# Kernel tuning notes

Hardware: AMD Instinct MI355X
Metric: run time of the kernel (lower is better)

Reference implementation:

```python
import jax, jax.numpy as jnp
import numpy as np

N = 50000
E = 800000
D = 128
H = 8
DH = D // H


def setup_inputs() -> dict:
    key = jax.random.key(0)
    ks = jax.random.split(key, 8)
    x = jax.random.normal(ks[0], (N, D), dtype=jnp.float32)
    src = jax.random.randint(ks[1], (E,), 0, N, dtype=jnp.int32)
    dst = jax.random.randint(ks[2], (E,), 0, N, dtype=jnp.int32)
    s = 1.0 / np.sqrt(D)
    w_qkv = jax.random.uniform(ks[3], (3 * D, D), jnp.float32, -s, s)
    b_qkv = jax.random.uniform(ks[4], (3 * D,), jnp.float32, -s, s)
    w_out = jax.random.uniform(ks[5], (D, D), jnp.float32, -s, s)
    b_out = jax.random.uniform(ks[6], (D,), jnp.float32, -s, s)
    return {"x": x, "src": src, "dst": dst, "w_qkv": w_qkv, "b_qkv": b_qkv,
            "w_out": w_out, "b_out": b_out}


def reference(x, src, dst, w_qkv, b_qkv, w_out, b_out):
    n = x.shape[0]
    coef = 1.0 / np.sqrt(DH)
    qkv = (x @ w_qkv.T + b_qkv).reshape(n, H, 3 * DH)
    q, k, v = qkv[..., :DH], qkv[..., DH:2 * DH], qkv[..., 2 * DH:]
    # per-edge scores: dot(k[src], q[dst]) per head -> [E, H]
    scores = jnp.einsum('ehd,ehd->eh', k[src], q[dst]) * coef
    # edge softmax over edges sharing the same destination node
    smax = jax.ops.segment_max(scores, dst, num_segments=n)  # [N, H]
    smax = jnp.where(jnp.isfinite(smax), smax, 0.0)
    ex = jnp.exp(scores - smax[dst])                          # [E, H]
    denom = jax.ops.segment_sum(ex, dst, num_segments=n)      # [N, H]
    probs = ex / jnp.maximum(denom[dst], 1e-30)
    # weighted aggregation of source values -> [N, H, DH]
    agg = jax.ops.segment_sum(probs[:, :, None] * v[src], dst, num_segments=n)
    out = agg.reshape(n, D) @ w_out.T + b_out
    return out
```

## Files before the change

kernel.cpp:

```cpp
#include <hip/hip_runtime.h>
#include <math.h>

#define DD   128
#define NQKV 384
#define CAP  128

typedef __attribute__((ext_vector_type(8))) short          bf16x8;
typedef __attribute__((ext_vector_type(8))) unsigned short ushort8;
typedef __attribute__((ext_vector_type(4))) float          f32x4;

__device__ __forceinline__ unsigned short f2bf(float f) {
    unsigned u = __float_as_uint(f);
    u += 0x7fffu + ((u >> 16) & 1u);
    return (unsigned short)(u >> 16);
}
__device__ __forceinline__ float bflo(unsigned u) { return __uint_as_float(u << 16); }
__device__ __forceinline__ float bfhi(unsigned u) { return __uint_as_float(u & 0xffff0000u); }

__device__ __forceinline__ unsigned char f2e4m3(float f) {
    float a = f * 0x1p-120f;
    unsigned u = __float_as_uint(a);
    unsigned s = (u >> 24) & 0x80u;
    u &= 0x7fffffffu;
    u += 0x7ffffu + ((u >> 20) & 1u);
    unsigned mag = u >> 20;
    if (mag > 0x7eu) mag = 0x7eu;
    return (unsigned char)(s | mag);
}
__device__ __forceinline__ float e4m3f(unsigned w, int k) {
    unsigned t = w << (24 - 8 * k);
    return __uint_as_float((t & 0x80000000u) | ((t & 0x7f000000u) >> 4));
}

#define NWQ8 (NQKV * DD / 8)
#define NWO8 (DD * DD / 8)

__global__ void prep_kernel(const float* __restrict__ x,
                            const float* __restrict__ w_qkv, const float* __restrict__ w_out,
                            unsigned short* __restrict__ xbf,
                            unsigned short* __restrict__ wqb, unsigned short* __restrict__ wob,
                            int* __restrict__ counts, int nzc4, int nx8) {
    int i = blockIdx.x * blockDim.x + threadIdx.x;
    if (i < nzc4) {
        ((int4*)counts)[i] = make_int4(0, 0, 0, 0);
        return;
    }
    int j = i - nzc4;
    const float* s;
    unsigned short* d;
    if (j < NWQ8)              { s = w_qkv + (size_t)j * 8; d = wqb + (size_t)j * 8; }
    else if (j < NWQ8 + NWO8)  { int k = j - NWQ8; s = w_out + (size_t)k * 8; d = wob + (size_t)k * 8; }
    else {
        int k = j - NWQ8 - NWO8;
        if (k >= nx8) return;
        s = x + (size_t)k * 8; d = xbf + (size_t)k * 8;
    }
    const float4* p = (const float4*)s;
    float4 a = p[0], b = p[1];
    float v[8] = {a.x, a.y, a.z, a.w, b.x, b.y, b.z, b.w};
    ushort8 vh;
    #pragma unroll
    for (int t = 0; t < 8; ++t) vh[t] = f2bf(v[t]);
    *(ushort8*)d = vh;
}

#define TM 128
#define TN 128
#define GY_QKV 170
#define GX_OUT 196

__global__ __launch_bounds__(256, 2) void scatter_qkv_kernel(
    const int* __restrict__ src, const int* __restrict__ dst,
    int* __restrict__ counts, int* __restrict__ lists, int E, int nsb,
    const unsigned short* __restrict__ Xb,
    const unsigned short* __restrict__ B,
    const float* __restrict__ bias, unsigned short* __restrict__ Cq,
    unsigned char* __restrict__ Ck8, unsigned short* __restrict__ Cv,
    int M, int mtiles)
{
    __shared__ unsigned short Bs[TN * DD];

    if ((int)blockIdx.x < nsb) {
        int t = blockIdx.x * blockDim.x + threadIdx.x;
        int base = t * 8;
        if (base >= E) return;
        if (base + 8 <= E) {
            int4 d0 = *(const int4*)(dst + base);
            int4 d1 = *(const int4*)(dst + base + 4);
            int4 s0 = *(const int4*)(src + base);
            int4 s1 = *(const int4*)(src + base + 4);
            int dd[8] = {d0.x, d0.y, d0.z, d0.w, d1.x, d1.y, d1.z, d1.w};
            int ss[8] = {s0.x, s0.y, s0.z, s0.w, s1.x, s1.y, s1.z, s1.w};
            int pos[8];
            #pragma unroll
            for (int i = 0; i < 8; ++i) pos[i] = atomicAdd(&counts[dd[i]], 1);
            #pragma unroll
            for (int i = 0; i < 8; ++i)
                if (pos[i] < CAP) lists[(size_t)dd[i] * CAP + pos[i]] = ss[i];
        } else {
            for (int e = base; e < E; ++e) {
                int d = dst[e];
                int pos = atomicAdd(&counts[d], 1);
                if (pos < CAP) lists[(size_t)d * CAP + pos] = src[e];
            }
        }
        return;
    }

    const int qb   = (int)blockIdx.x - nsb;
    const int tid  = threadIdx.x;
    const int l    = tid & 63;
    const int wv   = tid >> 6;
    const int quad = l >> 4;
    const int l15  = l & 15;
    const int wm   = (wv & 1) * 64;
    const int wn   = (wv >> 1) * 64;
    const int n0   = (qb % 3) * TN;
    const int mt_start = qb / 3;

    const size_t gbase = (size_t)n0 * DD;
    for (int i = tid; i < TN * 16; i += 256) {
        int col = i >> 4, g = i & 15;
        int gs  = g ^ (col & 15);
        *(ushort8*)&Bs[col * DD + gs * 8] = *(const ushort8*)(B + gbase + (size_t)col * DD + g * 8);
    }
    __syncthreads();

    for (int mt0 = mt_start; mt0 < mtiles; mt0 += GY_QKV) {
        const int m0 = mt0 * TM;

        f32x4 acc[4][4];
        #pragma unroll
        for (int i = 0; i < 4; ++i)
            #pragma unroll
            for (int j = 0; j < 4; ++j) acc[i][j] = (f32x4)0.f;

        bf16x8 af[4][4];
        #pragma unroll
        for (int mt = 0; mt < 4; ++mt) {
            const unsigned short* ar = Xb + (size_t)(m0 + wm + mt * 16 + l15) * DD + quad * 8;
            #pragma unroll
            for (int kq = 0; kq < 4; ++kq) af[mt][kq] = *(const bf16x8*)(ar + kq * 32);
        }

        #pragma unroll
        for (int kq = 0; kq < 4; ++kq) {
            bf16x8 bh[4];
            #pragma unroll
            for (int nt = 0; nt < 4; ++nt) {
                int colL = wn + nt * 16 + l15;
                int gs   = (kq * 4 + quad) ^ (colL & 15);
                bh[nt] = *(const bf16x8*)&Bs[colL * DD + gs * 8];
            }
            #pragma unroll
            for (int mt = 0; mt < 4; ++mt)
                #pragma unroll
                for (int nt = 0; nt < 4; ++nt)
                    acc[mt][nt] = __builtin_amdgcn_mfma_f32_16x16x32_bf16(af[mt][kq], bh[nt], acc[mt][nt], 0, 0, 0);
        }

        #pragma unroll
        for (int nt = 0; nt < 4; ++nt) {
            int j = n0 + wn + nt * 16 + l15;
            float bj = bias[j];
            int h = j / 48;
            int r = j - h * 48;
            int seg = (r >= 32) ? 2 : ((r >= 16) ? 1 : 0);
            int bc  = h * 16 + r - seg * 16;
            if (seg == 1) {
                #pragma unroll
                for (int mt = 0; mt < 4; ++mt)
                    #pragma unroll
                    for (int rr = 0; rr < 4; ++rr) {
                        int m = m0 + wm + mt * 16 + quad * 4 + rr;
                        if (m < M) Ck8[(size_t)m * DD + bc] = f2e4m3(acc[mt][nt][rr] + bj);
                    }
            } else {
                unsigned short* dstp = (seg == 0 ? Cq : Cv);
                #pragma unroll
                for (int mt = 0; mt < 4; ++mt)
                    #pragma unroll
                    for (int rr = 0; rr < 4; ++rr) {
                        int m = m0 + wm + mt * 16 + quad * 4 + rr;
                        if (m < M) dstp[(size_t)m * DD + bc] = f2bf(acc[mt][nt][rr] + bj);
                    }
            }
        }
    }
}

__global__ __launch_bounds__(256, 2) void out_gemm_kernel(
    const unsigned short* __restrict__ A,
    const unsigned short* __restrict__ B,
    const float* __restrict__ bias, float* __restrict__ C, int M, int mtiles)
{
    __shared__ unsigned short Bs[TN * DD];

    const int tid  = threadIdx.x;
    const int l    = tid & 63;
    const int wv   = tid >> 6;
    const int quad = l >> 4;
    const int l15  = l & 15;
    const int wm   = (wv & 1) * 64;
    const int wn   = (wv >> 1) * 64;

    for (int i = tid; i < TN * 16; i += 256) {
        int col = i >> 4, g = i & 15;
        int gs  = g ^ (col & 15);
        *(ushort8*)&Bs[col * DD + gs * 8] = *(const ushort8*)(B + (size_t)col * DD + g * 8);
    }
    __syncthreads();

    for (int mt0 = blockIdx.x; mt0 < mtiles; mt0 += gridDim.x) {
        const int m0 = mt0 * TM;

        f32x4 acc[4][4];
        #pragma unroll
        for (int i = 0; i < 4; ++i)
            #pragma unroll
            for (int j = 0; j < 4; ++j) acc[i][j] = (f32x4)0.f;

        bf16x8 af[4][4];
        #pragma unroll
        for (int mt = 0; mt < 4; ++mt) {
            const int mrow = m0 + wm + mt * 16 + l15;
            const int mclamp = (mrow < M) ? mrow : (M - 1);
            #pragma unroll
            for (int kq = 0; kq < 4; ++kq)
                af[mt][kq] = *(const bf16x8*)(A + (size_t)mclamp * DD + kq * 32 + quad * 8);
        }

        #pragma unroll
        for (int kq = 0; kq < 4; ++kq) {
            bf16x8 bh[4];
            #pragma unroll
            for (int nt = 0; nt < 4; ++nt) {
                int colL = wn + nt * 16 + l15;
                int gs   = (kq * 4 + quad) ^ (colL & 15);
                bh[nt] = *(const bf16x8*)&Bs[colL * DD + gs * 8];
            }
            #pragma unroll
            for (int mt = 0; mt < 4; ++mt)
                #pragma unroll
                for (int nt = 0; nt < 4; ++nt)
                    acc[mt][nt] = __builtin_amdgcn_mfma_f32_16x16x32_bf16(af[mt][kq], bh[nt], acc[mt][nt], 0, 0, 0);
        }

        #pragma unroll
        for (int nt = 0; nt < 4; ++nt) {
            int j = wn + nt * 16 + l15;
            float bj = bias[j];
            #pragma unroll
            for (int mt = 0; mt < 4; ++mt)
                #pragma unroll
                for (int rr = 0; rr < 4; ++rr) {
                    int m = m0 + wm + mt * 16 + quad * 4 + rr;
                    if (m < M) C[(size_t)m * DD + j] = acc[mt][nt][rr] + bj;
                }
        }
    }
}

#define ATTN_BLOCKS 2048

#define ATTN_STEP(cka, cvv, nka, nvv)                                             \
  {                                                                                \
    const int cnt  = min(8, deg - c);                                              \
    const bool more = (c + 8 < deg);                                               \
    const int nn = lists[row0 + min(c + 16 + e, deg - 1)];                         \
    if (more) {                                                                    \
      nka = *(const uint4*)(kb8 + ((((unsigned)nxt) << 7) + hoff));                \
      _Pragma("unroll")                                                            \
      for (int ee = 0; ee < 8; ++ee)                                               \
        nvv[ee] = *(const unsigned*)(vb8 + ((((unsigned)__shfl(nxt, ee)) << 8) + loff4)); \
    }                                                                              \
         \
    float sA = e4m3f(cka.x, 0) * q0.x;                                             \
    sA = fmaf(e4m3f(cka.x, 1), q0.y, sA);                                          \
    sA = fmaf(e4m3f(cka.x, 2), q0.z, sA);                                          \
    sA = fmaf(e4m3f(cka.x, 3), q0.w, sA);                                          \
    float sB = e4m3f(cka.y, 0) * q1.x;                                             \
    sB = fmaf(e4m3f(cka.y, 1), q1.y, sB);                                          \
    sB = fmaf(e4m3f(cka.y, 2), q1.z, sB);                                          \
    sB = fmaf(e4m3f(cka.y, 3), q1.w, sB);                                          \
    float sC = e4m3f(cka.z, 0) * q2.x;                                             \
    sC = fmaf(e4m3f(cka.z, 1), q2.y, sC);                                          \
    sC = fmaf(e4m3f(cka.z, 2), q2.z, sC);                                          \
    sC = fmaf(e4m3f(cka.z, 3), q2.w, sC);                                          \
    float sD = e4m3f(cka.w, 0) * q3.x;                                             \
    sD = fmaf(e4m3f(cka.w, 1), q3.y, sD);                                          \
    sD = fmaf(e4m3f(cka.w, 2), q3.z, sD);                                          \
    sD = fmaf(e4m3f(cka.w, 3), q3.w, sD);                                          \
    const float s_ = (sA + sB) + (sC + sD);                                        \
    const float pp = __expf(s_ * 0.25f);                           \
    const float p_ = (e < cnt) ? pp : 0.f;                                         \
    l_run += p_;                                                                   \
    _Pragma("unroll")                                                              \
    for (int ee = 0; ee < 8; ++ee) {                                               \
      const float pe = __shfl(p_, lbase | ee);          \
      if ((ee & 1) == 0) {                                                         \
        acc0a = fmaf(pe, bflo(cvv[ee]), acc0a);                                    \
        acc1a = fmaf(pe, bfhi(cvv[ee]), acc1a);                                    \
      } else {                                                                     \
        acc0b = fmaf(pe, bflo(cvv[ee]), acc0b);                                    \
        acc1b = fmaf(pe, bfhi(cvv[ee]), acc1b);                                    \
      }                                                                            \
    }                                                                              \
    nxt = nn;                                                                      \
    c += 8;                                                                        \
  }

__global__ __launch_bounds__(256) void wave_attn_kernel(
    const unsigned short* __restrict__ qbf, const unsigned char* __restrict__ k8,
    const unsigned short* __restrict__ vbf, const int* __restrict__ lists,
    const int* __restrict__ counts,
    unsigned short* __restrict__ agg, int N)
{
    const int lane   = threadIdx.x & 63;
    const int wid    = blockIdx.x * 4 + (threadIdx.x >> 6);
    const int nwaves = gridDim.x * 4;

    const int h = lane >> 3;
    const int e = lane & 7;
    const unsigned hoff  = (unsigned)h << 4;
    const unsigned loff4 = (unsigned)lane << 2;
    const int lbase = lane & 0x38;

    const char* kb8 = (const char*)k8;
    const char* vb8 = (const char*)vbf;
    const char* qb8 = (const char*)qbf;
    char*       ab8 = (char*)agg;

    for (int n = wid; n < N; n += nwaves) {
        const int deg = min(counts[n], CAP);
        const unsigned ooff = (((unsigned)n) << 8) + loff4;
        if (deg == 0) {
            *(unsigned*)(ab8 + ooff) = 0u;
            continue;
        }

        const int row0 = n * CAP;

        const unsigned qoff = (((unsigned)n) << 8) + ((unsigned)h << 5);
        const uint4 qa = *(const uint4*)(qb8 + qoff);
        const uint4 qb = *(const uint4*)(qb8 + qoff + 16);
        const float S = 0x1p120f;
        const float4 q0 = make_float4(bflo(qa.x)*S, bfhi(qa.x)*S, bflo(qa.y)*S, bfhi(qa.y)*S);
        const float4 q1 = make_float4(bflo(qa.z)*S, bfhi(qa.z)*S, bflo(qa.w)*S, bfhi(qa.w)*S);
        const float4 q2 = make_float4(bflo(qb.x)*S, bfhi(qb.x)*S, bflo(qb.y)*S, bfhi(qb.y)*S);
        const float4 q3 = make_float4(bflo(qb.z)*S, bfhi(qb.z)*S, bflo(qb.w)*S, bfhi(qb.w)*S);

        const int c0s = lists[row0 + min(e, deg - 1)];
        int nxt = lists[row0 + min(8 + e, deg - 1)];

        uint4 ka0, ka1;
        unsigned vv0[8], vv1[8];
        {
            ka0 = *(const uint4*)(kb8 + ((((unsigned)c0s) << 7) + hoff));
            #pragma unroll
            for (int ee = 0; ee < 8; ++ee)
                vv0[ee] = *(const unsigned*)(vb8 + ((((unsigned)__shfl(c0s, ee)) << 8) + loff4));
        }
        ka1 = ka0;
        #pragma unroll
        for (int ee = 0; ee < 8; ++ee) vv1[ee] = 0u;

        float l_run = 0.f;
        float acc0a = 0.f, acc0b = 0.f, acc1a = 0.f, acc1b = 0.f;

        int c = 0;
        for (;;) {
            ATTN_STEP(ka0, vv0, ka1, vv1);
            if (c >= deg) break;
            ATTN_STEP(ka1, vv1, ka0, vv0);
            if (c >= deg) break;
        }

        l_run += __shfl_xor(l_run, 1);
        l_run += __shfl_xor(l_run, 2);
        l_run += __shfl_xor(l_run, 4);

        const float inv = 1.f / fmaxf(l_run, 1e-30f);
        const float o0 = (acc0a + acc0b) * inv, o1 = (acc1a + acc1b) * inv;
        *(unsigned*)(ab8 + ooff) = (unsigned)f2bf(o0) | ((unsigned)f2bf(o1) << 16);
    }
}

extern "C" void kernel_launch(void* const* d_in, const int* in_sizes, int n_in,
                              void* d_out, int out_size, void* d_ws, size_t ws_size,
                              hipStream_t stream) {
    const float* x     = (const float*)d_in[0];
    const int*   src   = (const int*)  d_in[1];
    const int*   dst   = (const int*)  d_in[2];
    const float* w_qkv = (const float*)d_in[3];
    const float* b_qkv = (const float*)d_in[4];
    const float* w_out = (const float*)d_in[5];
    const float* b_out = (const float*)d_in[6];
    float* out = (float*)d_out;

    const int N = in_sizes[0] / DD;
    const int E = in_sizes[1];

    typedef unsigned short u16;
    char* ws = (char*)d_ws;
    u16* qbf   = (u16*)ws;           ws += (size_t)N * DD * sizeof(u16);
    unsigned char* k8 = (unsigned char*)ws; ws += (size_t)N * DD;
    u16* vbf   = (u16*)ws;           ws += (size_t)N * DD * sizeof(u16);
    u16* aggb  = (u16*)ws;           ws += (size_t)N * DD * sizeof(u16);
    u16* wqb   = (u16*)ws;           ws += (size_t)NQKV * DD * sizeof(u16);
    u16* wob   = (u16*)ws;           ws += (size_t)DD * DD * sizeof(u16);
    int* counts = (int*)ws;          ws += (size_t)((N + 3) / 4 * 4) * sizeof(int);
    int* lists  = (int*)ws;          ws += (size_t)N * CAP * sizeof(int);

    u16* xbf = aggb;

    const int nx8  = N * DD / 8;
    const int nzc4 = (N + 3) / 4;
    const int npb  = (nzc4 + NWQ8 + NWO8 + nx8 + 255) / 256;
    const int nsb  = ((E + 7) / 8 + 255) / 256;
    const int MB   = (N + TM - 1) / TM;

    prep_kernel<<<npb, 256, 0, stream>>>(x, w_qkv, w_out, xbf, wqb, wob,
                                         counts, nzc4, nx8);
    scatter_qkv_kernel<<<nsb + 3 * GY_QKV, 256, 0, stream>>>(
        src, dst, counts, lists, E, nsb,
        xbf, wqb, b_qkv, qbf, k8, vbf, N, MB);

    wave_attn_kernel<<<ATTN_BLOCKS, 256, 0, stream>>>(
        qbf, k8, vbf, lists, counts, aggb, N);

    out_gemm_kernel<<<GX_OUT, 256, 0, stream>>>(
        aggb, wob, b_out, out, N, MB);
}
```

Baseline: 211.0 us.

## Store edge lists as 16-bit indices and interleave scatter with QKV GEMM blocks

Adjacency lists now hold unsigned short source indices instead of int, halving list writes in the scatter and reads in the attention kernel. Block indices of the fused scatter/QKV launch are remapped so each group of 16 blocks has 7 scatter and 9 GEMM blocks, so atomic scatter work runs concurrently with GEMM tiles rather than all first. The 16-bit indices assume N fits in 65535.

```diff
diff --git a/kernel.cpp b/kernel.cpp
--- a/kernel.cpp
+++ b/kernel.cpp
@@ -71,7 +71,7 @@
 
 __global__ __launch_bounds__(256, 2) void scatter_qkv_kernel(
     const int* __restrict__ src, const int* __restrict__ dst,
-    int* __restrict__ counts, int* __restrict__ lists, int E, int nsb,
+    int* __restrict__ counts, unsigned short* __restrict__ lists, int E, int nsb,
     const unsigned short* __restrict__ Xb,
     const unsigned short* __restrict__ B,
     const float* __restrict__ bias, unsigned short* __restrict__ Cq,
@@ -80,8 +80,12 @@
 {
     __shared__ unsigned short Bs[TN * DD];
 
-    if ((int)blockIdx.x < nsb) {
-        int t = blockIdx.x * blockDim.x + threadIdx.x;
+    const int grp = (int)blockIdx.x >> 4;
+    const int rr_ = (int)blockIdx.x & 15;
+    if (rr_ < 7) {
+        const int sblk = grp * 7 + rr_;
+        if (sblk >= nsb) return;
+        int t = sblk * 256 + (int)threadIdx.x;
         int base = t * 8;
         if (base >= E) return;
         if (base + 8 <= E) {
@@ -96,18 +100,19 @@
             for (int i = 0; i < 8; ++i) pos[i] = atomicAdd(&counts[dd[i]], 1);
             #pragma unroll
             for (int i = 0; i < 8; ++i)
-                if (pos[i] < CAP) lists[(size_t)dd[i] * CAP + pos[i]] = ss[i];
+                if (pos[i] < CAP) lists[(size_t)dd[i] * CAP + pos[i]] = (unsigned short)ss[i];
         } else {
             for (int e = base; e < E; ++e) {
                 int d = dst[e];
                 int pos = atomicAdd(&counts[d], 1);
-                if (pos < CAP) lists[(size_t)d * CAP + pos] = src[e];
+                if (pos < CAP) lists[(size_t)d * CAP + pos] = (unsigned short)src[e];
             }
         }
         return;
     }
 
-    const int qb   = (int)blockIdx.x - nsb;
+    const int qb = grp * 9 + (rr_ - 7);
+    if (qb >= 3 * GY_QKV) return;
     const int tid  = threadIdx.x;
     const int l    = tid & 63;
     const int wv   = tid >> 6;
@@ -267,7 +272,7 @@
   {                                                                                \
     const int cnt  = min(8, deg - c);                                              \
     const bool more = (c + 8 < deg);                                               \
-    const int nn = lists[row0 + min(c + 16 + e, deg - 1)];                         \
+    const int nn = (int)lists[row0 + min(c + 16 + e, deg - 1)];                    \
     if (more) {                                                                    \
       nka = *(const uint4*)(kb8 + ((((unsigned)nxt) << 7) + hoff));                \
       _Pragma("unroll")                                                            \
@@ -312,7 +317,7 @@
 
 __global__ __launch_bounds__(256) void wave_attn_kernel(
     const unsigned short* __restrict__ qbf, const unsigned char* __restrict__ k8,
-    const unsigned short* __restrict__ vbf, const int* __restrict__ lists,
+    const unsigned short* __restrict__ vbf, const unsigned short* __restrict__ lists,
     const int* __restrict__ counts,
     unsigned short* __restrict__ agg, int N)
 {
@@ -350,8 +355,8 @@
         const float4 q2 = make_float4(bflo(qb.x)*S, bfhi(qb.x)*S, bflo(qb.y)*S, bfhi(qb.y)*S);
         const float4 q3 = make_float4(bflo(qb.z)*S, bfhi(qb.z)*S, bflo(qb.w)*S, bfhi(qb.w)*S);
 
-        const int c0s = lists[row0 + min(e, deg - 1)];
-        int nxt = lists[row0 + min(8 + e, deg - 1)];
+        const int c0s = (int)lists[row0 + min(e, deg - 1)];
+        int nxt       = (int)lists[row0 + min(8 + e, deg - 1)];
 
         uint4 ka0, ka1;
         unsigned vv0[8], vv1[8];
@@ -410,7 +415,7 @@
     u16* wqb   = (u16*)ws;           ws += (size_t)NQKV * DD * sizeof(u16);
     u16* wob   = (u16*)ws;           ws += (size_t)DD * DD * sizeof(u16);
     int* counts = (int*)ws;          ws += (size_t)((N + 3) / 4 * 4) * sizeof(int);
-    int* lists  = (int*)ws;          ws += (size_t)N * CAP * sizeof(int);
+    u16* lists  = (u16*)ws;          ws += (size_t)N * CAP * sizeof(u16);
 
     u16* xbf = aggb;
 
@@ -419,10 +424,12 @@
     const int npb  = (nzc4 + NWQ8 + NWO8 + nx8 + 255) / 256;
     const int nsb  = ((E + 7) / 8 + 255) / 256;
     const int MB   = (N + TM - 1) / TM;
+    const int NQB  = 3 * GY_QKV;
+    const int ngrp = max((nsb + 6) / 7, (NQB + 8) / 9);
 
     prep_kernel<<<npb, 256, 0, stream>>>(x, w_qkv, w_out, xbf, wqb, wob,
                                          counts, nzc4, nx8);
-    scatter_qkv_kernel<<<nsb + 3 * GY_QKV, 256, 0, stream>>>(
+    scatter_qkv_kernel<<<ngrp * 16, 256, 0, stream>>>(
         src, dst, counts, lists, E, nsb,
         xbf, wqb, b_qkv, qbf, k8, vbf, N, MB);
 
```

After: 200.4 us. 1.05x faster.
